# Optimization experiments

Measured on AMD Instinct MI355X. Metric: run time of the kernel, lower is better.

Reference implementation:

```python
import jax, jax.numpy as jnp
import numpy as np

EPS = 1e-08

def setup_inputs() -> dict:
    key = jax.random.key(0)
    ks = jax.random.split(key, 6)
    B, IN_C, OUT_C, H, W, STYLE_DIM = 16, 64, 64, 128, 128, 512
    x = jax.random.normal(ks[0], (B, IN_C, H, W), dtype=jnp.float32)
    style = jax.random.normal(ks[1], (B, STYLE_DIM), dtype=jnp.float32)
    # weight: (1, out_c, in_c, ks, ks) with kernel_size=1, kaiming-like scale
    fan_in = IN_C * 1 * 1
    gain = np.sqrt(2.0 / (1.0 + 0.2 ** 2))
    weight = jax.random.normal(ks[2], (1, OUT_C, IN_C, 1, 1), dtype=jnp.float32) * (gain / np.sqrt(fan_in))
    bias = jnp.zeros((1, OUT_C), dtype=jnp.float32)
    # geo_feature: Linear(style_dim, in_c)
    geo_w = jax.random.normal(ks[3], (IN_C, STYLE_DIM), dtype=jnp.float32) * (np.sqrt(2.0 / (1.0 + 0.2 ** 2)) / np.sqrt(STYLE_DIM))
    geo_b = jnp.zeros((IN_C,), dtype=jnp.float32)
    return {"x": x, "style": style, "weight": weight, "bias": bias, "geo_w": geo_w, "geo_b": geo_b}

def reference(x, style, weight, bias, geo_w, geo_b):
    # x: (b, in_c, h, w); style: (b, style_dim)
    # geo_feature linear -> (b, in_c), modulation factor (style + 1)
    s = style @ geo_w.T + geo_b                      # (b, in_c)
    mod = s + 1.0
    # per-sample modulated weight: (b, out_c, in_c, 1, 1) -> (b, out_c, in_c)
    w = weight[:, :, :, 0, 0] * mod[:, None, :]       # (b, out_c, in_c)
    # demodulate over (in_c, kh, kw)
    demod = jax.lax.rsqrt(jnp.sum(w * w, axis=2) + EPS)  # (b, out_c)
    w = w * demod[:, :, None]
    # groups=batch 1x1 conv == per-sample channel mixing
    out = jnp.einsum('boi,bihw->bohw', w, x)          # (b, out_c, h, w)
    out = out + bias[0][None, :, None, None]
    return out
```

## Files before the change

kernel.cpp:

```cpp
#include <hip/hip_runtime.h>
#include <hip/hip_bf16.h>

#define B_SZ 16
#define IN_C 64
#define OUT_C 64
#define STYLE_DIM 512
#define HW 16384
#define HWT 256
#define EPS 1e-8f

__global__ __launch_bounds__(256) void fused_kernel(
    const float* __restrict__ x,
    const float* __restrict__ style,
    const float* __restrict__ weight,
    const float* __restrict__ bias,
    const float* __restrict__ geo_w,
    const float* __restrict__ geo_b,
    float* __restrict__ out)
{
    __shared__ float smod[IN_C];
    __shared__ float sWT[IN_C * OUT_C];

    const int tid = threadIdx.x;
    const int b   = blockIdx.x >> 6;
    const int hwt = (blockIdx.x & 63) * HWT;

    {
        const int i    = tid >> 2;
        const int part = tid & 3;
        const float4* st4 = reinterpret_cast<const float4*>(style + b * STYLE_DIM + part * 128);
        const float4* gw4 = reinterpret_cast<const float4*>(geo_w + i * STYLE_DIM + part * 128);
        float s = 0.0f;
        #pragma unroll
        for (int k = 0; k < 32; ++k) {
            const float4 a = st4[k];
            const float4 g = gw4[k];
            s = fmaf(a.x, g.x, s); s = fmaf(a.y, g.y, s);
            s = fmaf(a.z, g.z, s); s = fmaf(a.w, g.w, s);
        }
        s += __shfl_xor(s, 1);
        s += __shfl_xor(s, 2);
        if (part == 0) smod[i] = s + geo_b[i] + 1.0f;
    }
    __syncthreads();

    if (tid < OUT_C) {
        const int o = tid;
        const float* wr = weight + o * IN_C;
        float d = 0.0f;
        #pragma unroll
        for (int ii = 0; ii < IN_C; ++ii) {
            const float wv = wr[ii] * smod[ii];
            d = fmaf(wv, wv, d);
        }
        d = rsqrtf(d + EPS);
        #pragma unroll
        for (int ii = 0; ii < IN_C; ++ii)
            sWT[ii * OUT_C + o] = wr[ii] * smod[ii] * d;
    }
    __syncthreads();

    const int obase = (tid >> 5) << 3;
    const int hw    = hwt + (tid & 31) * 8;

    const float* xb = x + (size_t)b * IN_C * HW + hw;

    float acc[8][8];
    #pragma unroll
    for (int o = 0; o < 8; ++o)
        #pragma unroll
        for (int h = 0; h < 8; ++h) acc[o][h] = 0.0f;

#define FMA_TILE(W0, W1, XA, XC) do {                                   \
        const float wv[8] = {(W0).x,(W0).y,(W0).z,(W0).w,               \
                             (W1).x,(W1).y,(W1).z,(W1).w};              \
        const float xv[8] = {(XA).x,(XA).y,(XA).z,(XA).w,               \
                             (XC).x,(XC).y,(XC).z,(XC).w};              \
        _Pragma("unroll")                                               \
        for (int o = 0; o < 8; ++o)                                     \
            _Pragma("unroll")                                           \
            for (int h = 0; h < 8; ++h)                                 \
                acc[o][h] = fmaf(wv[o], xv[h], acc[o][h]);              \
    } while (0)

    float4 ca0 = *reinterpret_cast<const float4*>(xb);
    float4 cc0 = *reinterpret_cast<const float4*>(xb + 4);
    float4 ca1 = *reinterpret_cast<const float4*>(xb + HW);
    float4 cc1 = *reinterpret_cast<const float4*>(xb + HW + 4);

    #pragma unroll
    for (int i = 0; i < IN_C; i += 2) {
        float4 na0 = ca0, nc0 = cc0, na1 = ca1, nc1 = cc1;
        if (i + 2 < IN_C) {
            na0 = *reinterpret_cast<const float4*>(xb + (size_t)(i + 2) * HW);
            nc0 = *reinterpret_cast<const float4*>(xb + (size_t)(i + 2) * HW + 4);
            na1 = *reinterpret_cast<const float4*>(xb + (size_t)(i + 3) * HW);
            nc1 = *reinterpret_cast<const float4*>(xb + (size_t)(i + 3) * HW + 4);
        }
        const float4 w0 = *reinterpret_cast<const float4*>(&sWT[i * OUT_C + obase]);
        const float4 w1 = *reinterpret_cast<const float4*>(&sWT[i * OUT_C + obase + 4]);
        FMA_TILE(w0, w1, ca0, cc0);
        const float4 u0 = *reinterpret_cast<const float4*>(&sWT[(i + 1) * OUT_C + obase]);
        const float4 u1 = *reinterpret_cast<const float4*>(&sWT[(i + 1) * OUT_C + obase + 4]);
        FMA_TILE(u0, u1, ca1, cc1);
        ca0 = na0; cc0 = nc0; ca1 = na1; cc1 = nc1;
    }
#undef FMA_TILE

    float* ob = out + ((size_t)b * OUT_C + obase) * HW + hw;
    #pragma unroll
    for (int o = 0; o < 8; ++o) {
        const float bv = bias[obase + o];
        float4 r0, r1;
        r0.x = acc[o][0] + bv;  r0.y = acc[o][1] + bv;
        r0.z = acc[o][2] + bv;  r0.w = acc[o][3] + bv;
        r1.x = acc[o][4] + bv;  r1.y = acc[o][5] + bv;
        r1.z = acc[o][6] + bv;  r1.w = acc[o][7] + bv;
        *reinterpret_cast<float4*>(ob + (size_t)o * HW)     = r0;
        *reinterpret_cast<float4*>(ob + (size_t)o * HW + 4) = r1;
    }
}

extern "C" void kernel_launch(void* const* d_in, const int* in_sizes, int n_in,
                              void* d_out, int out_size, void* d_ws, size_t ws_size,
                              hipStream_t stream) {
    const float* x      = (const float*)d_in[0];
    const float* style  = (const float*)d_in[1];
    const float* weight = (const float*)d_in[2];
    const float* bias   = (const float*)d_in[3];
    const float* geo_w  = (const float*)d_in[4];
    const float* geo_b  = (const float*)d_in[5];
    float* out = (float*)d_out;

    fused_kernel<<<B_SZ * (HW / HWT), 256, 0, stream>>>(
        x, style, weight, bias, geo_w, geo_b, out);
}
```

Measured before the change: 169.6 us.

## Stage x tiles through double-buffered LDS and parallelize demodulation across all threads

New measurement: 175.8 us. 1.04x slower.

```diff
diff --git a/kernel.cpp b/kernel.cpp
--- a/kernel.cpp
+++ b/kernel.cpp
@@ -20,10 +20,18 @@
 {
     __shared__ float smod[IN_C];
     __shared__ float sWT[IN_C * OUT_C];
+    __shared__ float xs[2][8][HWT];
 
     const int tid = threadIdx.x;
     const int b   = blockIdx.x >> 6;
     const int hwt = (blockIdx.x & 63) * HWT;
+
+    const int sch = tid >> 5;
+    const int shw = (tid & 31) * 4;
+    const float* xgb = x + ((size_t)b * IN_C + sch) * HW + hwt;
+
+    float4 sa = *reinterpret_cast<const float4*>(xgb + shw);
+    float4 sb = *reinterpret_cast<const float4*>(xgb + 128 + shw);
 
     {
         const int i    = tid >> 2;
@@ -44,26 +52,35 @@
     }
     __syncthreads();
 
-    if (tid < OUT_C) {
-        const int o = tid;
-        const float* wr = weight + o * IN_C;
+    {
+        const int o    = tid >> 2;
+        const int part = tid & 3;
+        const float* wr = weight + o * IN_C + part * 16;
+        const float* sm = smod + part * 16;
+        float wv[16];
         float d = 0.0f;
         #pragma unroll
-        for (int ii = 0; ii < IN_C; ++ii) {
-            const float wv = wr[ii] * smod[ii];
-            d = fmaf(wv, wv, d);
+        for (int k = 0; k < 16; ++k) {
+            wv[k] = wr[k] * sm[k];
+            d = fmaf(wv[k], wv[k], d);
         }
+        d += __shfl_xor(d, 1);
+        d += __shfl_xor(d, 2);
         d = rsqrtf(d + EPS);
         #pragma unroll
-        for (int ii = 0; ii < IN_C; ++ii)
-            sWT[ii * OUT_C + o] = wr[ii] * smod[ii] * d;
+        for (int k = 0; k < 16; ++k)
+            sWT[(part * 16 + k) * OUT_C + o] = wv[k] * d;
+    }
+
+    {
+        float* dst = &xs[0][sch][0];
+        *reinterpret_cast<float4*>(dst + shw)       = sa;
+        *reinterpret_cast<float4*>(dst + 128 + shw) = sb;
     }
     __syncthreads();
 
-    const int obase = (tid >> 5) << 3;
-    const int hw    = hwt + (tid & 31) * 8;
-
-    const float* xb = x + (size_t)b * IN_C * HW + hw;
+    const int og  = (tid >> 5) * 8;
+    const int hwg = (tid & 31) * 4;
 
     float acc[8][8];
     #pragma unroll
@@ -71,53 +88,63 @@
         #pragma unroll
         for (int h = 0; h < 8; ++h) acc[o][h] = 0.0f;
 
-#define FMA_TILE(W0, W1, XA, XC) do {                                   \
-        const float wv[8] = {(W0).x,(W0).y,(W0).z,(W0).w,               \
-                             (W1).x,(W1).y,(W1).z,(W1).w};              \
-        const float xv[8] = {(XA).x,(XA).y,(XA).z,(XA).w,               \
-                             (XC).x,(XC).y,(XC).z,(XC).w};              \
-        _Pragma("unroll")                                               \
-        for (int o = 0; o < 8; ++o)                                     \
-            _Pragma("unroll")                                           \
-            for (int h = 0; h < 8; ++h)                                 \
-                acc[o][h] = fmaf(wv[o], xv[h], acc[o][h]);              \
+#define COMPUTE_CHUNK(BUF, C0) do {                                          \
+        _Pragma("unroll")                                                    \
+        for (int cc = 0; cc < 8; ++cc) {                                     \
+            const float4 xa = *reinterpret_cast<const float4*>(&xs[BUF][cc][hwg]);        \
+            const float4 xc = *reinterpret_cast<const float4*>(&xs[BUF][cc][128 + hwg]);  \
+            const float4 w0 = *reinterpret_cast<const float4*>(&sWT[((C0) + cc) * OUT_C + og]);     \
+            const float4 w1 = *reinterpret_cast<const float4*>(&sWT[((C0) + cc) * OUT_C + og + 4]); \
+            const float wv[8] = {w0.x, w0.y, w0.z, w0.w, w1.x, w1.y, w1.z, w1.w};        \
+            const float xv[8] = {xa.x, xa.y, xa.z, xa.w, xc.x, xc.y, xc.z, xc.w};        \
+            _Pragma("unroll")                                                \
+            for (int o = 0; o < 8; ++o)                                      \
+                _Pragma("unroll")                                            \
+                for (int h = 0; h < 8; ++h)                                  \
+                    acc[o][h] = fmaf(wv[o], xv[h], acc[o][h]);               \
+        }                                                                    \
     } while (0)
 
-    float4 ca0 = *reinterpret_cast<const float4*>(xb);
-    float4 cc0 = *reinterpret_cast<const float4*>(xb + 4);
-    float4 ca1 = *reinterpret_cast<const float4*>(xb + HW);
-    float4 cc1 = *reinterpret_cast<const float4*>(xb + HW + 4);
+    for (int c2 = 0; c2 < 4; ++c2) {
+        const int cB = 2 * c2 + 1;
+        {
+            const float* src = xgb + (size_t)cB * 8 * HW;
+            sa = *reinterpret_cast<const float4*>(src + shw);
+            sb = *reinterpret_cast<const float4*>(src + 128 + shw);
+        }
+        COMPUTE_CHUNK(0, 2 * c2 * 8);
+        {
+            float* dst = &xs[1][sch][0];
+            *reinterpret_cast<float4*>(dst + shw)       = sa;
+            *reinterpret_cast<float4*>(dst + 128 + shw) = sb;
+        }
+        __syncthreads();
+        if (c2 < 3) {
+            const float* src = xgb + (size_t)(cB + 1) * 8 * HW;
+            sa = *reinterpret_cast<const float4*>(src + shw);
+            sb = *reinterpret_cast<const float4*>(src + 128 + shw);
+        }
+        COMPUTE_CHUNK(1, cB * 8);
+        if (c2 < 3) {
+            float* dst = &xs[0][sch][0];
+            *reinterpret_cast<float4*>(dst + shw)       = sa;
+            *reinterpret_cast<float4*>(dst + 128 + shw) = sb;
+            __syncthreads();
+        }
+    }
+#undef COMPUTE_CHUNK
 
-    #pragma unroll
-    for (int i = 0; i < IN_C; i += 2) {
-        float4 na0 = ca0, nc0 = cc0, na1 = ca1, nc1 = cc1;
-        if (i + 2 < IN_C) {
-            na0 = *reinterpret_cast<const float4*>(xb + (size_t)(i + 2) * HW);
-            nc0 = *reinterpret_cast<const float4*>(xb + (size_t)(i + 2) * HW + 4);
-            na1 = *reinterpret_cast<const float4*>(xb + (size_t)(i + 3) * HW);
-            nc1 = *reinterpret_cast<const float4*>(xb + (size_t)(i + 3) * HW + 4);
-        }
-        const float4 w0 = *reinterpret_cast<const float4*>(&sWT[i * OUT_C + obase]);
-        const float4 w1 = *reinterpret_cast<const float4*>(&sWT[i * OUT_C + obase + 4]);
-        FMA_TILE(w0, w1, ca0, cc0);
-        const float4 u0 = *reinterpret_cast<const float4*>(&sWT[(i + 1) * OUT_C + obase]);
-        const float4 u1 = *reinterpret_cast<const float4*>(&sWT[(i + 1) * OUT_C + obase + 4]);
-        FMA_TILE(u0, u1, ca1, cc1);
-        ca0 = na0; cc0 = nc0; ca1 = na1; cc1 = nc1;
-    }
-#undef FMA_TILE
-
-    float* ob = out + ((size_t)b * OUT_C + obase) * HW + hw;
+    float* ob = out + ((size_t)b * OUT_C + og) * HW + hwt;
     #pragma unroll
     for (int o = 0; o < 8; ++o) {
-        const float bv = bias[obase + o];
+        const float bv = bias[og + o];
         float4 r0, r1;
         r0.x = acc[o][0] + bv;  r0.y = acc[o][1] + bv;
         r0.z = acc[o][2] + bv;  r0.w = acc[o][3] + bv;
         r1.x = acc[o][4] + bv;  r1.y = acc[o][5] + bv;
         r1.z = acc[o][6] + bv;  r1.w = acc[o][7] + bv;
-        *reinterpret_cast<float4*>(ob + (size_t)o * HW)     = r0;
-        *reinterpret_cast<float4*>(ob + (size_t)o * HW + 4) = r1;
+        *reinterpret_cast<float4*>(ob + (size_t)o * HW + hwg)       = r0;
+        *reinterpret_cast<float4*>(ob + (size_t)o * HW + 128 + hwg) = r1;
     }
 }
 
```
